# Performance work log

Measured on AMD Instinct MI355X. Metric: run time of the kernel, lower is better.

The kernel has to match this reference:

```python
import jax, jax.numpy as jnp
import numpy as np
import math

L, B, T, C, H, DH, V, MEM = 6, 2, 1024, 1024, 16, 64, 32000, 128

def _ln(x, g, b):
    m = jnp.mean(x, -1, keepdims=True)
    v = jnp.mean((x - m) ** 2, -1, keepdims=True)
    return (x - m) * jax.lax.rsqrt(v + 1e-5) * g + b

def _rel_shift(x):
    # x: [B,H,Q,K]; TransformerXL shift trick: pad zero col, reshape, drop first row
    b, h, q, k = x.shape
    xp = jnp.pad(x, ((0, 0), (0, 0), (0, 0), (1, 0)))
    xp = xp.reshape(b, h, k + 1, q)
    return xp[:, :, 1:, :].reshape(b, h, q, k)

def setup_inputs():
    key = jax.random.key(0)
    ks = jax.random.split(key, 12)
    d = {}
    d['idx'] = jax.random.randint(ks[0], (B, T), 0, V)
    d['mems'] = jax.random.normal(ks[1], (L, B, MEM, C), dtype=jnp.float32) * 0.02
    d['wte'] = jax.random.normal(ks[2], (V, C), dtype=jnp.float32) * 0.02
    d['ln1_g'] = jnp.ones((L, C), jnp.float32); d['ln1_b'] = jnp.zeros((L, C), jnp.float32)
    d['attn_w'] = jax.random.normal(ks[3], (L, C, 3 * C), dtype=jnp.float32) * 0.02
    d['attn_b'] = jnp.zeros((L, 3 * C), jnp.float32)
    d['proj_w'] = jax.random.normal(ks[4], (L, C, C), dtype=jnp.float32) * 0.02
    d['proj_b'] = jnp.zeros((L, C), jnp.float32)
    d['r_emb'] = jax.random.normal(ks[5], (L, H, DH), dtype=jnp.float32) * 0.02
    d['r_bias'] = jax.random.normal(ks[6], (L, H, DH), dtype=jnp.float32) * 0.02
    d['ln2_g'] = jnp.ones((L, C), jnp.float32); d['ln2_b'] = jnp.zeros((L, C), jnp.float32)
    d['fc_w'] = jax.random.normal(ks[7], (L, C, 4 * C), dtype=jnp.float32) * 0.02
    d['fc_b'] = jnp.zeros((L, 4 * C), jnp.float32)
    d['fc2_w'] = jax.random.normal(ks[8], (L, 4 * C, C), dtype=jnp.float32) * 0.02
    d['fc2_b'] = jnp.zeros((L, C), jnp.float32)
    d['lnf_g'] = jnp.ones((C,), jnp.float32); d['lnf_b'] = jnp.zeros((C,), jnp.float32)
    d['lm_w'] = jax.random.normal(ks[9], (C, V), dtype=jnp.float32) * 0.02
    return d

def _attn(x, mem, w, b, pw, pb, remb, rbias):
    Bx, Tx, Cx = x.shape
    cat = jnp.concatenate([mem, x], axis=1)          # [B,K,C], K = mem_len + Tx
    K = cat.shape[1]
    qkv = cat @ w + b
    q, k, v = jnp.split(qkv, 3, axis=-1)
    q = q.reshape(Bx, K, H, DH).transpose(0, 2, 1, 3)
    k = k.reshape(Bx, K, H, DH).transpose(0, 2, 1, 3)
    v = v.reshape(Bx, K, H, DH).transpose(0, 2, 1, 3)
    q = q + rbias[None, :, None, :]
    AC = jnp.einsum('bhid,bhjd->bhij', q, k)
    # BD: r is r_emb broadcast over positions, so q@r^T is constant over j
    s = jnp.einsum('bhid,hd->bhi', q, remb)
    BD = _rel_shift(jnp.broadcast_to(s[..., None], (Bx, H, K, K)))
    p = jax.nn.softmax((AC + BD) / math.sqrt(DH), axis=-1)
    y = jnp.einsum('bhij,bhjd->bhid', p, v).transpose(0, 2, 1, 3).reshape(Bx, K, Cx)
    y = y @ pw + pb
    new_mem = cat[:, -MEM:]
    return y, new_mem

def reference(idx, mems, wte, ln1_g, ln1_b, attn_w, attn_b, proj_w, proj_b, r_emb, r_bias, ln2_g, ln2_b, fc_w, fc_b, fc2_w, fc2_b, lnf_g, lnf_b, lm_w):
    x = wte[idx]                                      # [B,T,C]
    new_mems = []
    for l in range(L):
        h = _ln(x, ln1_g[l], ln1_b[l])
        y, nm = _attn(h, mems[l], attn_w[l], attn_b[l], proj_w[l], proj_b[l], r_emb[l], r_bias[l])
        h2 = _ln(y, ln2_g[l], ln2_b[l])
        m = jax.nn.gelu(h2 @ fc_w[l] + fc_b[l], approximate=False) @ fc2_w[l] + fc2_b[l]
        x = y + m                                     # note: residual onto attn output (length grows by MEM per layer)
        new_mems.append(nm)
    x = _ln(x, lnf_g, lnf_b)
    logits = x @ lm_w                                 # [B, L*MEM+T, V]
    return logits, jnp.stack(new_mems)
```

## Files before the change

### kernel.cpp

```cpp
#include <hip/hip_runtime.h>
#include <hip/hip_bf16.h>
#include <hip/hip_fp16.h>

#define LNUM 6
#define BB 2
#define TT 1024
#define CC 1024
#define HH 16
#define DHH 64
#define VV 32000
#define MM 128

typedef _Float16 f16;
typedef _Float16 f16x8 __attribute__((ext_vector_type(8)));
typedef float f32x4 __attribute__((ext_vector_type(4)));

__device__ __forceinline__ void g2lds16(const void* g, void* l) {
    __builtin_amdgcn_global_load_lds((const __attribute__((address_space(1))) void*)g,
                                     (__attribute__((address_space(3))) void*)l,
                                     16, 0, 0);
}

__device__ __forceinline__ float wred(float v) {
#pragma unroll
    for (int o = 32; o > 0; o >>= 1) v += __shfl_xor(v, o);
    return v;
}

__global__ __launch_bounds__(256)
void transpose_k(const float* __restrict__ W, f16* __restrict__ WT, int R, int Cc)
{
    __shared__ float tile[64][65];
    const size_t base = (size_t)blockIdx.z * R * Cc;
    const int c0 = blockIdx.x * 64, r0 = blockIdx.y * 64;
    const int tx = threadIdx.x & 15, ty = threadIdx.x >> 4;
#pragma unroll
    for (int i = 0; i < 4; ++i) {
        const int row = ty + i * 16;
        float4 v = *(const float4*)&W[base + (size_t)(r0 + row) * Cc + c0 + tx * 4];
        tile[row][tx * 4 + 0] = v.x;
        tile[row][tx * 4 + 1] = v.y;
        tile[row][tx * 4 + 2] = v.z;
        tile[row][tx * 4 + 3] = v.w;
    }
    __syncthreads();
#pragma unroll
    for (int i = 0; i < 4; ++i) {
        const int c = ty + i * 16;
        union { f16 h4[4]; uint2 u; } pk;
        pk.h4[0] = (f16)tile[tx * 4 + 0][c];
        pk.h4[1] = (f16)tile[tx * 4 + 1][c];
        pk.h4[2] = (f16)tile[tx * 4 + 2][c];
        pk.h4[3] = (f16)tile[tx * 4 + 3][c];
        *(uint2*)&WT[base + (size_t)(c0 + c) * R + r0 + tx * 4] = pk.u;
    }
}

__global__ __launch_bounds__(256)
void embed_k(const int* __restrict__ idx, const float* __restrict__ wte, float* __restrict__ X)
{
    const int row = blockIdx.x;
    const int id = idx[row];
    const float4* src = (const float4*)(wte + (size_t)id * CC);
    float4* dst = (float4*)(X + (size_t)row * CC);
    dst[threadIdx.x] = src[threadIdx.x];
}

__global__ __launch_bounds__(256)
void ln_k(const float* __restrict__ X, const float* __restrict__ g,
          const float* __restrict__ bta, f16* __restrict__ outH)
{
    const int row = blockIdx.x * 4 + (threadIdx.x >> 6);
    const int lane = threadIdx.x & 63;
    const float4* xr = (const float4*)(X + (size_t)row * CC);
    float4 v[4];
    float s = 0.f;
#pragma unroll
    for (int i = 0; i < 4; ++i) { v[i] = xr[i * 64 + lane]; s += v[i].x + v[i].y + v[i].z + v[i].w; }
    s = wred(s);
    const float mean = s * (1.f / CC);
    float q = 0.f;
#pragma unroll
    for (int i = 0; i < 4; ++i) {
        float a = v[i].x - mean, b = v[i].y - mean, c = v[i].z - mean, d = v[i].w - mean;
        q += a * a + b * b + c * c + d * d;
    }
    q = wred(q);
    const float rs = rsqrtf(q * (1.f / CC) + 1e-5f);
    const float4* g4 = (const float4*)g;
    const float4* b4 = (const float4*)bta;
    uint2* orow = (uint2*)(outH + (size_t)row * CC);
#pragma unroll
    for (int i = 0; i < 4; ++i) {
        float4 gg = g4[i * 64 + lane], bb = b4[i * 64 + lane];
        union { f16 h4[4]; uint2 u; } pk;
        pk.h4[0] = (f16)((v[i].x - mean) * rs * gg.x + bb.x);
        pk.h4[1] = (f16)((v[i].y - mean) * rs * gg.y + bb.y);
        pk.h4[2] = (f16)((v[i].z - mean) * rs * gg.z + bb.z);
        pk.h4[3] = (f16)((v[i].w - mean) * rs * gg.w + bb.w);
        orow[i * 64 + lane] = pk.u;
    }
}

__global__ __launch_bounds__(256)
void ln1cat_k(const float* __restrict__ X, const float* __restrict__ memsL,
              const float* __restrict__ g, const float* __restrict__ bta,
              f16* __restrict__ catH, float* __restrict__ nmOut,
              int K, int Kin)
{
    const int row = blockIdx.x * 4 + (threadIdx.x >> 6);
    const int lane = threadIdx.x & 63;
    const int b = row / K, rr = row % K;
    uint2* crow = (uint2*)(catH + (size_t)row * CC);
    if (rr < MM) {
        const float4* src = (const float4*)(memsL + ((size_t)b * MM + rr) * CC);
#pragma unroll
        for (int i = 0; i < 4; ++i) {
            float4 vv = src[i * 64 + lane];
            union { f16 h4[4]; uint2 u; } pk;
            pk.h4[0] = (f16)vv.x; pk.h4[1] = (f16)vv.y; pk.h4[2] = (f16)vv.z; pk.h4[3] = (f16)vv.w;
            crow[i * 64 + lane] = pk.u;
        }
        return;
    }
    const float4* xr = (const float4*)(X + ((size_t)b * Kin + (rr - MM)) * CC);
    float4 v[4];
    float s = 0.f;
#pragma unroll
    for (int i = 0; i < 4; ++i) { v[i] = xr[i * 64 + lane]; s += v[i].x + v[i].y + v[i].z + v[i].w; }
    s = wred(s);
    const float mean = s * (1.f / CC);
    float q = 0.f;
#pragma unroll
    for (int i = 0; i < 4; ++i) {
        float a = v[i].x - mean, b2 = v[i].y - mean, c = v[i].z - mean, d = v[i].w - mean;
        q += a * a + b2 * b2 + c * c + d * d;
    }
    q = wred(q);
    const float rs = rsqrtf(q * (1.f / CC) + 1e-5f);
    const float4* g4 = (const float4*)g;
    const float4* b4 = (const float4*)bta;
    float4* nm = nullptr;
    if (rr >= K - MM) nm = (float4*)(nmOut + ((size_t)b * MM + (rr - (K - MM))) * CC);
#pragma unroll
    for (int i = 0; i < 4; ++i) {
        float4 gg = g4[i * 64 + lane], bb = b4[i * 64 + lane];
        float4 o;
        o.x = (v[i].x - mean) * rs * gg.x + bb.x;
        o.y = (v[i].y - mean) * rs * gg.y + bb.y;
        o.z = (v[i].z - mean) * rs * gg.z + bb.z;
        o.w = (v[i].w - mean) * rs * gg.w + bb.w;
        union { f16 h4[4]; uint2 u; } pk;
        pk.h4[0] = (f16)o.x; pk.h4[1] = (f16)o.y; pk.h4[2] = (f16)o.z; pk.h4[3] = (f16)o.w;
        crow[i * 64 + lane] = pk.u;
        if (nm) nm[i * 64 + lane] = o;
    }
}

template <int EPI>
__global__ __launch_bounds__(256, 2)
void gemm_k(const f16* __restrict__ A, const f16* __restrict__ BT,
            const float* __restrict__ bias, const float* __restrict__ res,
            float* __restrict__ outF, f16* __restrict__ outH,
            int M, int N, int Kc)
{
    __shared__ f16 sA[2][128 * 32];
    __shared__ f16 sB[2][128 * 32];

    const int nbn = N >> 7;
    const int nwg = gridDim.x;
    const int id = blockIdx.x;
    const int qq = nwg >> 3, r8 = nwg & 7;
    const int xcd = id & 7, pos = id >> 3;
    const int wgid = (xcd < r8 ? xcd * (qq + 1) : r8 * (qq + 1) + (xcd - r8) * qq) + pos;
    const int bm = wgid / nbn, bn = wgid % nbn;

    const int tid = threadIdx.x;
    const int w = tid >> 6, l = tid & 63;
    const int wr = w >> 1, wc = w & 1;
    const int lr = l & 15, lk = (l >> 4) * 8;

    f32x4 acc[4][4] = {};

    const int ar = w * 32 + (l >> 2);
    const int ak = (l & 3) * 8;
    const f16* gA = A + (size_t)(bm * 128 + ar) * Kc + ak;
    const f16* gB = BT + (size_t)(bn * 128 + ar) * Kc + ak;

    auto stage = [&](int slot, int kt) {
        g2lds16(gA + kt, &sA[slot][w * 1024]);
        g2lds16(gA + kt + (size_t)16 * Kc, &sA[slot][w * 1024 + 512]);
        g2lds16(gB + kt, &sB[slot][w * 1024]);
        g2lds16(gB + kt + (size_t)16 * Kc, &sB[slot][w * 1024 + 512]);
    };

    stage(0, 0);
    asm volatile("s_waitcnt vmcnt(0)" ::: "memory");
    __builtin_amdgcn_s_barrier();

    int cur = 0;
    for (int kt = 0; kt < Kc; kt += 32) {
        if (kt + 32 < Kc) stage(cur ^ 1, kt + 32);
        f16x8 af[4], bf[4];
#pragma unroll
        for (int mi = 0; mi < 4; ++mi) af[mi] = *(const f16x8*)&sA[cur][(wr * 64 + mi * 16 + lr) * 32 + lk];
#pragma unroll
        for (int ni = 0; ni < 4; ++ni) bf[ni] = *(const f16x8*)&sB[cur][(wc * 64 + ni * 16 + lr) * 32 + lk];
        asm volatile("s_waitcnt lgkmcnt(0)" ::: "memory");
        __builtin_amdgcn_sched_barrier(0);
#pragma unroll
        for (int mi = 0; mi < 4; ++mi)
#pragma unroll
            for (int ni = 0; ni < 4; ++ni)
                acc[mi][ni] = __builtin_amdgcn_mfma_f32_16x16x32_f16(af[mi], bf[ni], acc[mi][ni], 0, 0, 0);
        asm volatile("s_waitcnt vmcnt(0)" ::: "memory");
        __builtin_amdgcn_s_barrier();
        cur ^= 1;
    }

    const int orow0 = bm * 128 + wr * 64 + (l >> 4) * 4;
    const int ocol0 = bn * 128 + wc * 64 + lr;
#pragma unroll
    for (int mi = 0; mi < 4; ++mi)
#pragma unroll
        for (int ni = 0; ni < 4; ++ni) {
            const int col = ocol0 + ni * 16;
            const float bv = (EPI >= 1) ? bias[col] : 0.f;
#pragma unroll
            for (int r = 0; r < 4; ++r) {
                const int row = orow0 + mi * 16 + r;
                float v = acc[mi][ni][r] + bv;
                if (EPI == 2) {
                    const float u = 1.5957691216057308f * (v + 0.044715f * v * v * v);
                    const float e = __expf(u);
                    v = v * e / (e + 1.f);
                    outH[(size_t)row * N + col] = (f16)v;
                } else if (EPI == 4) {
                    outH[(size_t)row * N + col] = (f16)v;
                } else if (EPI == 3) {
                    v += res[(size_t)row * N + col];
                    outF[(size_t)row * N + col] = v;
                } else {
                    outF[(size_t)row * N + col] = v;
                }
            }
        }
}

template <int EPI>
__global__ __launch_bounds__(512, 2)
void gemm256_k(const f16* __restrict__ A, const f16* __restrict__ BT,
               const float* __restrict__ bias,
               float* __restrict__ outF, f16* __restrict__ outH,
               int M, int N, int Kc)
{
    __shared__ char ldsbuf[131072];
    char* ldsA = ldsbuf;
    char* ldsB = ldsbuf + 65536;

    const int nbm = M >> 8;
    const int nwg = gridDim.x;
    int id = blockIdx.x;
    const int qq = nwg >> 3, rr8 = nwg & 7;
    const int xcd = id & 7, pos = id >> 3;
    const int wgid = (xcd < rr8 ? xcd * (qq + 1) : rr8 * (qq + 1) + (xcd - rr8) * qq) + pos;
    const int bm = wgid % nbm, bn = wgid / nbm;

    const int t_ = threadIdx.x;
    const int w = t_ >> 6, l = t_ & 63;
    const int wm = w >> 2, wn = w & 3;
    const int lr = l & 15, lhi = l >> 4;

    const f16* gA = A + (size_t)bm * 256 * Kc;
    const f16* gB = BT + (size_t)bn * 256 * Kc;

    auto stage = [&](const f16* Gbase, char* ldsHalf, int kt) {
#pragma unroll
        for (int ii = 0; ii < 2; ++ii) {
            const int gb = (w << 1) + ii;
            const int s = (gb << 6) + l;
            const int row = s >> 3, grp = s & 7;
            g2lds16(Gbase + (size_t)row * Kc + kt + ((grp ^ (row & 7)) << 3),
                    ldsHalf + gb * 1024);
        }
    };
    auto rdfrag = [&](const char* halfBase, int rowInHalf, int ks) -> f16x8 {
        return *(const f16x8*)(halfBase + rowInHalf * 128 +
                               ((((ks << 2) + lhi) ^ (rowInHalf & 7)) << 4));
    };

    f32x4 acc[8][4] = {};
    f16x8 aA[4][2], blo[2][2], bhi[2][2];

    const int NT = Kc >> 6;
    const char* aHalf0 = ldsA + wm * 16384;
    const char* aHalf1 = ldsA + 32768 + wm * 16384;
    const char* bHalf0 = ldsB + (wn >> 1) * 16384;
    const char* bHalf1 = ldsB + 32768 + (wn >> 1) * 16384;
    const int brow = (wn & 1) * 64;

    stage(gA, ldsA + 0, 0);
    stage(gA + (size_t)128 * Kc, ldsA + 16384, 0);
    stage(gB, ldsB + 0, 0);
    stage(gB + (size_t)128 * Kc, ldsB + 16384, 0);
    stage(gB, ldsB + 32768, 64);
    stage(gB + (size_t)128 * Kc, ldsB + 49152, 64);
    asm volatile("s_waitcnt vmcnt(0)" ::: "memory");
    __builtin_amdgcn_s_barrier();

#define MFMA_QUAD(MQ, NQ, BR)                                                            \
    __builtin_amdgcn_s_setprio(1);                                                       \
    _Pragma("unroll") for (int mf = 0; mf < 4; ++mf)                                     \
    _Pragma("unroll") for (int nf = 0; nf < 2; ++nf)                                     \
    _Pragma("unroll") for (int ks = 0; ks < 2; ++ks)                                     \
        acc[(MQ)*4 + mf][(NQ)*2 + nf] =                                                  \
            __builtin_amdgcn_mfma_f32_16x16x32_f16(aA[mf][ks], BR[nf][ks],               \
                                                   acc[(MQ)*4 + mf][(NQ)*2 + nf], 0, 0, 0); \
    __builtin_amdgcn_s_setprio(0);

#define PHASE_SYNC()                                          \
    __builtin_amdgcn_s_barrier();                             \
    asm volatile("s_waitcnt lgkmcnt(0)" ::: "memory");        \
    __builtin_amdgcn_sched_barrier(0);

    for (int t = 0; t < NT; t += 2) {
        const bool pf0 = (t + 2) < NT;
        const int kb = (t + 1) << 6, kc2 = (t + 2) << 6, kd = (t + 3) << 6;

#pragma unroll
        for (int mf = 0; mf < 4; ++mf)
#pragma unroll
            for (int ks = 0; ks < 2; ++ks) aA[mf][ks] = rdfrag(aHalf0, mf * 16 + lr, ks);
#pragma unroll
        for (int nf = 0; nf < 2; ++nf)
#pragma unroll
            for (int ks = 0; ks < 2; ++ks) blo[nf][ks] = rdfrag(bHalf0, brow + nf * 16 + lr, ks);
        stage(gA, ldsA + 32768, kb);
        PHASE_SYNC();
        MFMA_QUAD(0, 0, blo);
        __builtin_amdgcn_s_barrier();

#pragma unroll
        for (int nf = 0; nf < 2; ++nf)
#pragma unroll
            for (int ks = 0; ks < 2; ++ks) bhi[nf][ks] = rdfrag(bHalf0, brow + 32 + nf * 16 + lr, ks);
        stage(gA + (size_t)128 * Kc, ldsA + 49152, kb);
        PHASE_SYNC();
        MFMA_QUAD(0, 1, bhi);
        __builtin_amdgcn_s_barrier();

#pragma unroll
        for (int mf = 0; mf < 4; ++mf)
#pragma unroll
            for (int ks = 0; ks < 2; ++ks) aA[mf][ks] = rdfrag(aHalf0, 64 + mf * 16 + lr, ks);
        if (pf0) stage(gB, ldsB + 0, kc2);
        PHASE_SYNC();
        MFMA_QUAD(1, 0, blo);
        __builtin_amdgcn_s_barrier();

        if (pf0) {
            stage(gB + (size_t)128 * Kc, ldsB + 16384, kc2);
            asm volatile("s_waitcnt vmcnt(4)" ::: "memory");
        } else {
            asm volatile("s_waitcnt vmcnt(0)" ::: "memory");
        }
        PHASE_SYNC();
        MFMA_QUAD(1, 1, bhi);
        __builtin_amdgcn_s_barrier();

#pragma unroll
        for (int mf = 0; mf < 4; ++mf)
#pragma unroll
            for (int ks = 0; ks < 2; ++ks) aA[mf][ks] = rdfrag(aHalf1, mf * 16 + lr, ks);
#pragma unroll
        for (int nf = 0; nf < 2; ++nf)
#pragma unroll
            for (int ks = 0; ks < 2; ++ks) blo[nf][ks] = rdfrag(bHalf1, brow + nf * 16 + lr, ks);
        if (pf0) stage(gA, ldsA + 0, kc2);
        PHASE_SYNC();
        MFMA_QUAD(0, 0, blo);
        __builtin_amdgcn_s_barrier();

#pragma unroll
        for (int nf = 0; nf < 2; ++nf)
#pragma unroll
            for (int ks = 0; ks < 2; ++ks) bhi[nf][ks] = rdfrag(bHalf1, brow + 32 + nf * 16 + lr, ks);
        if (pf0) stage(gA + (size_t)128 * Kc, ldsA + 16384, kc2);
        PHASE_SYNC();
        MFMA_QUAD(0, 1, bhi);
        __builtin_amdgcn_s_barrier();

#pragma unroll
        for (int mf = 0; mf < 4; ++mf)
#pragma unroll
            for (int ks = 0; ks < 2; ++ks) aA[mf][ks] = rdfrag(aHalf1, 64 + mf * 16 + lr, ks);
        if (pf0) stage(gB, ldsB + 32768, kd);
        PHASE_SYNC();
        MFMA_QUAD(1, 0, blo);
        __builtin_amdgcn_s_barrier();

        if (pf0) {
            stage(gB + (size_t)128 * Kc, ldsB + 49152, kd);
            asm volatile("s_waitcnt vmcnt(4)" ::: "memory");
        } else {
            asm volatile("s_waitcnt vmcnt(0)" ::: "memory");
        }
        PHASE_SYNC();
        MFMA_QUAD(1, 1, bhi);
        __builtin_amdgcn_s_barrier();
    }
#undef MFMA_QUAD
#undef PHASE_SYNC

    const int rb0 = bm * 256 + wm * 128 + lhi * 4;
    const int cb0 = bn * 256 + wn * 64 + lr;
#pragma unroll
    for (int mf = 0; mf < 8; ++mf)
#pragma unroll
        for (int nf = 0; nf < 4; ++nf) {
            const int col = cb0 + nf * 16;
            const float bv = (EPI >= 1) ? bias[col] : 0.f;
#pragma unroll
            for (int r = 0; r < 4; ++r) {
                const int row = rb0 + mf * 16 + r;
                float v = acc[mf][nf][r] + bv;
                if (EPI == 2) {
                    const float u = 1.5957691216057308f * (v + 0.044715f * v * v * v);
                    const float e = __expf(u);
                    v = v * e / (e + 1.f);
                    outH[(size_t)row * N + col] = (f16)v;
                } else if (EPI == 4) {
                    outH[(size_t)row * N + col] = (f16)v;
                } else {
                    __builtin_nontemporal_store(v, &outF[(size_t)row * N + col]);
                }
            }
        }
}

__global__ __launch_bounds__(256)
void attn_k(const f16* __restrict__ qkv, const float* __restrict__ remb,
            const float* __restrict__ rbias, f16* __restrict__ yH, int K)
{
    __shared__ f16 K_lds[2][64 * 64];
    __shared__ f16 Vt_lds[2][64 * 64];
    __shared__ f16 P_lds[64 * 64];
    __shared__ float s_s[66];

    const int b = blockIdx.x >> 4, h = blockIdx.x & 15;
    const int i0 = blockIdx.y * 64;
    const int t = threadIdx.x;
    const int w = t >> 6, l = t & 63;
    const int c = l & 15, g = l >> 4;

    const f16* qg = qkv + (size_t)b * K * 3072 + h * 64;
    const f16* kg = qg + 1024;
    const f16* vg = qg + 2048;
    const float* rb = rbias + h * 64;
    const float* re = remb + h * 64;

    const int kb = t >> 4, db = t & 15;

    auto stageK = [&](int j0, int slot) {
#pragma unroll
        for (int i = 0; i < 2; ++i) {
            const int s = w * 128 + i * 64 + l;
            const int row = s >> 3, grp = s & 7;
            g2lds16(kg + (size_t)(j0 + row) * 3072 + ((grp ^ (row & 7)) * 8),
                    (char*)K_lds[slot] + (size_t)(w * 128 + i * 64) * 16);
        }
    };
    auto loadV = [&](int j0, uint2* rowv) {
#pragma unroll
        for (int i = 0; i < 4; ++i)
            rowv[i] = *(const uint2*)(vg + (size_t)(j0 + kb * 4 + i) * 3072 + db * 4);
    };
    auto writeVt = [&](const uint2* rowvu, int slot) {
#pragma unroll
        for (int j = 0; j < 4; ++j) {
            union { uint2 u; f16 hh[4]; } colv;
#pragma unroll
            for (int i = 0; i < 4; ++i) {
                union { uint2 u; f16 hh[4]; } rv; rv.u = rowvu[i];
                colv.hh[i] = rv.hh[j];
            }
            const int d = db * 4 + j;
            *(uint2*)((char*)Vt_lds[slot] + d * 128 + ((kb * 8) ^ ((d & 7) << 4))) = colv.u;
        }
    };

    f16x8 qf[2];
    {
        const int qrow = i0 + w * 16 + c;
#pragma unroll
        for (int ks = 0; ks < 2; ++ks) {
            f16x8 raw = *(const f16x8*)(qg + (size_t)qrow * 3072 + ks * 32 + g * 8);
            f16x8 o;
#pragma unroll
            for (int j = 0; j < 8; ++j) o[j] = (f16)((float)raw[j] + rb[ks * 32 + g * 8 + j]);
            qf[ks] = o;
        }
    }
    if (t < 65) {
        float sv = 0.f;
        const int i = i0 + t;
        if (i < K) {
            const f16* qr = qg + (size_t)i * 3072;
#pragma unroll
            for (int d8 = 0; d8 < 8; ++d8) {
                f16x8 v8 = *(const f16x8*)(qr + d8 * 8);
#pragma unroll
                for (int j = 0; j < 8; ++j) sv += ((float)v8[j] + rb[d8 * 8 + j]) * re[d8 * 8 + j];
            }
        }
        s_s[t] = sv;
    }

    {
        uint2 rowv[4];
        stageK(0, 0);
        loadV(0, rowv);
        writeVt(rowv, 0);
    }
    __syncthreads();

    float sA[4], sB[4];
#pragma unroll
    for (int r = 0; r < 4; ++r) {
        sA[r] = s_s[w * 16 + g * 4 + r];
        sB[r] = s_s[w * 16 + g * 4 + r + 1];
    }

    float m_run[4] = {0.f, 0.f, 0.f, 0.f};
    float psum[4] = {0.f, 0.f, 0.f, 0.f};
    f32x4 yacc[4] = {};

    int cur = 0;
    for (int j0 = 0; j0 < K; j0 += 64, cur ^= 1) {
        const bool more = (j0 + 64) < K;
        uint2 rowv[4];
        if (more) { stageK(j0 + 64, cur ^ 1); loadV(j0 + 64, rowv); }

        f32x4 sc[4] = {};
#pragma unroll
        for (int tt = 0; tt < 4; ++tt) {
            const int row = tt * 16 + c;
#pragma unroll
            for (int ks = 0; ks < 2; ++ks) {
                f16x8 kf = *(const f16x8*)((char*)K_lds[cur] + row * 128 + ((ks * 64 + g * 16) ^ ((row & 7) << 4)));
                sc[tt] = __builtin_amdgcn_mfma_f32_16x16x32_f16(qf[ks], kf, sc[tt], 0, 0, 0);
            }
        }

        float p[4][4];
#pragma unroll
        for (int tt = 0; tt < 4; ++tt)
#pragma unroll
            for (int r = 0; r < 4; ++r) {
                const int gi = i0 + w * 16 + g * 4 + r;
                const int gj = j0 + tt * 16 + c;
                const float bd = (gj <= gi) ? sA[r] : ((gj == gi + 1) ? 0.f : sB[r]);
                p[tt][r] = (sc[tt][r] + bd) * 0.125f;
            }

        float lmax[4];
        bool need = false;
#pragma unroll
        for (int r = 0; r < 4; ++r) {
            lmax[r] = fmaxf(fmaxf(p[0][r], p[1][r]), fmaxf(p[2][r], p[3][r]));
            need |= (lmax[r] > m_run[r] + 8.f);
        }
        if (__any(need)) {
#pragma unroll
            for (int r = 0; r < 4; ++r) {
                float mx = lmax[r];
                mx = fmaxf(mx, __shfl_xor(mx, 1));
                mx = fmaxf(mx, __shfl_xor(mx, 2));
                mx = fmaxf(mx, __shfl_xor(mx, 4));
                mx = fmaxf(mx, __shfl_xor(mx, 8));
                if (mx > m_run[r]) {
                    const float f = __expf(m_run[r] - mx);
                    m_run[r] = mx;
                    psum[r] *= f;
#pragma unroll
                    for (int tt = 0; tt < 4; ++tt) yacc[tt][r] *= f;
                }
            }
        }
#pragma unroll
        for (int r = 0; r < 4; ++r) {
            float ss = 0.f;
#pragma unroll
            for (int tt = 0; tt < 4; ++tt) {
                const float e = __expf(p[tt][r] - m_run[r]);
                p[tt][r] = e;
                ss += e;
            }
            psum[r] += ss;
        }

        if (more) writeVt(rowv, cur ^ 1);
#pragma unroll
        for (int tt = 0; tt < 4; ++tt)
#pragma unroll
            for (int r = 0; r < 4; ++r) {
                const int q = w * 16 + g * 4 + r;
                *(f16*)((char*)P_lds + q * 128 + (((tt * 16 + c) * 2) ^ ((q & 7) << 4))) = (f16)p[tt][r];
            }
        asm volatile("s_waitcnt lgkmcnt(0)" ::: "memory");
        __builtin_amdgcn_sched_barrier(0);

        {
            const int qrow = w * 16 + c;
            f16x8 pa[2];
#pragma unroll
            for (int ks = 0; ks < 2; ++ks)
                pa[ks] = *(const f16x8*)((char*)P_lds + qrow * 128 + ((ks * 64 + g * 16) ^ ((qrow & 7) << 4)));
#pragma unroll
            for (int tt = 0; tt < 4; ++tt) {
                const int drow = tt * 16 + c;
#pragma unroll
                for (int ks = 0; ks < 2; ++ks) {
                    f16x8 vb = *(const f16x8*)((char*)Vt_lds[cur] + drow * 128 + ((ks * 64 + g * 16) ^ ((drow & 7) << 4)));
                    yacc[tt] = __builtin_amdgcn_mfma_f32_16x16x32_f16(pa[ks], vb, yacc[tt], 0, 0, 0);
                }
            }
        }
        __syncthreads();
    }

#pragma unroll
    for (int r = 0; r < 4; ++r) {
        float ps = psum[r];
        ps += __shfl_xor(ps, 1);
        ps += __shfl_xor(ps, 2);
        ps += __shfl_xor(ps, 4);
        ps += __shfl_xor(ps, 8);
        const float inv = 1.f / ps;
        const int row = i0 + w * 16 + g * 4 + r;
        f16* dst = yH + (size_t)(b * K + row) * CC + h * 64;
#pragma unroll
        for (int tt = 0; tt < 4; ++tt)
            dst[tt * 16 + c] = (f16)(yacc[tt][r] * inv);
    }
}

extern "C" void kernel_launch(void* const* d_in, const int* in_sizes, int n_in,
                              void* d_out, int out_size, void* d_ws, size_t ws_size,
                              hipStream_t stream)
{
    (void)in_sizes; (void)n_in; (void)out_size; (void)ws_size;
    const int*   idx    = (const int*)  d_in[0];
    const float* mems   = (const float*)d_in[1];
    const float* wte    = (const float*)d_in[2];
    const float* ln1_g  = (const float*)d_in[3];
    const float* ln1_b  = (const float*)d_in[4];
    const float* attn_w = (const float*)d_in[5];
    const float* attn_b = (const float*)d_in[6];
    const float* proj_w = (const float*)d_in[7];
    const float* proj_b = (const float*)d_in[8];
    const float* r_emb  = (const float*)d_in[9];
    const float* r_bias = (const float*)d_in[10];
    const float* ln2_g  = (const float*)d_in[11];
    const float* ln2_b  = (const float*)d_in[12];
    const float* fc_w   = (const float*)d_in[13];
    const float* fc_b   = (const float*)d_in[14];
    const float* fc2_w  = (const float*)d_in[15];
    const float* fc2_b  = (const float*)d_in[16];
    const float* lnf_g  = (const float*)d_in[17];
    const float* lnf_b  = (const float*)d_in[18];
    const float* lm_w   = (const float*)d_in[19];
    float* out = (float*)d_out;

    char* wp = (char*)d_ws; size_t off = 0;
    auto carve = [&](size_t bytes) -> void* {
        void* p = wp + off; off += (bytes + 255) & ~(size_t)255; return p;
    };
    const int KMAX = TT + LNUM * MM;
    f16*  attn_wT = (f16*) carve((size_t)LNUM * 3 * CC * CC * 2);
    f16*  proj_wT = (f16*) carve((size_t)LNUM * CC * CC * 2);
    f16*  fc_wT   = (f16*) carve((size_t)LNUM * 4 * CC * CC * 2);
    f16*  fc2_wT  = (f16*) carve((size_t)LNUM * 4 * CC * CC * 2);
    f16*  lm_wT   = (f16*) carve((size_t)VV * CC * 2);
    float* x0     = (float*)carve((size_t)BB * KMAX * CC * 4);
    float* x1     = (float*)carve((size_t)BB * KMAX * CC * 4);
    f16*  catH    = (f16*) carve((size_t)BB * KMAX * CC * 2);
    f16*  qkv16   = (f16*) carve((size_t)BB * KMAX * 3 * CC * 2);
    f16*  yH      = (f16*) carve((size_t)BB * KMAX * CC * 2);
    float* yp     = (float*)carve((size_t)BB * KMAX * CC * 4);
    f16*  h2H     = (f16*) carve((size_t)BB * KMAX * CC * 2);
    f16*  a1H     = (f16*) carve((size_t)BB * KMAX * 4 * CC * 2);
    f16*  xfH     = (f16*) carve((size_t)BB * KMAX * CC * 2);

    transpose_k<<<dim3(3 * CC / 64, CC / 64, LNUM), 256, 0, stream>>>(attn_w, attn_wT, CC, 3 * CC);
    transpose_k<<<dim3(CC / 64, CC / 64, LNUM),     256, 0, stream>>>(proj_w, proj_wT, CC, CC);
    transpose_k<<<dim3(4 * CC / 64, CC / 64, LNUM), 256, 0, stream>>>(fc_w, fc_wT, CC, 4 * CC);
    transpose_k<<<dim3(CC / 64, 4 * CC / 64, LNUM), 256, 0, stream>>>(fc2_w, fc2_wT, 4 * CC, CC);
    transpose_k<<<dim3(VV / 64, CC / 64, 1),        256, 0, stream>>>(lm_w, lm_wT, CC, VV);

    embed_k<<<BB * TT, 256, 0, stream>>>(idx, wte, x0);

    const size_t LOGITS = (size_t)BB * KMAX * VV;
    float* xcur = x0; float* xnxt = x1;
    for (int l = 0; l < LNUM; ++l) {
        const int Kin = TT + MM * l;
        const int K = Kin + MM;
        const int Mrows = BB * K;
        const int nbm128 = Mrows / 128;
        ln1cat_k<<<Mrows / 4, 256, 0, stream>>>(xcur, mems + (size_t)l * BB * MM * CC,
                                                ln1_g + l * CC, ln1_b + l * CC,
                                                catH, out + LOGITS + (size_t)l * BB * MM * CC, K, Kin);
        gemm_k<4><<<(3 * CC / 128) * nbm128, 256, 0, stream>>>(
            catH, attn_wT + (size_t)l * 3 * CC * CC, attn_b + (size_t)l * 3 * CC, nullptr,
            nullptr, qkv16, Mrows, 3 * CC, CC);
        attn_k<<<dim3(BB * HH, K / 64), 256, 0, stream>>>(
            qkv16, r_emb + (size_t)l * HH * DHH, r_bias + (size_t)l * HH * DHH, yH, K);
        gemm_k<1><<<(CC / 128) * nbm128, 256, 0, stream>>>(
            yH, proj_wT + (size_t)l * CC * CC, proj_b + (size_t)l * CC, nullptr,
            yp, nullptr, Mrows, CC, CC);
        ln_k<<<Mrows / 4, 256, 0, stream>>>(yp, ln2_g + l * CC, ln2_b + l * CC, h2H);
        gemm_k<2><<<(4 * CC / 128) * nbm128, 256, 0, stream>>>(
            h2H, fc_wT + (size_t)l * 4 * CC * CC, fc_b + (size_t)l * 4 * CC, nullptr,
            nullptr, a1H, Mrows, 4 * CC, CC);
        gemm_k<3><<<(CC / 128) * nbm128, 256, 0, stream>>>(
            a1H, fc2_wT + (size_t)l * 4 * CC * CC, fc2_b + (size_t)l * CC, yp,
            xnxt, nullptr, Mrows, CC, 4 * CC);
        float* tmp = xcur; xcur = xnxt; xnxt = tmp;
    }
    ln_k<<<(BB * KMAX) / 4, 256, 0, stream>>>(xcur, lnf_g, lnf_b, xfH);
    gemm256_k<0><<<(BB * KMAX / 256) * (VV / 256), 512, 0, stream>>>(
        xfH, lm_wT, nullptr, out, nullptr, BB * KMAX, VV, CC);
}
```

Before: 2.029 ms.

## Deepen gemm K-tile to 64 with XOR-swizzled LDS layout

The 128x128 gemm kernel now stages 64-wide K slices instead of 32. This halves the number of barrier and wait iterations and doubles the MFMA work issued per sync. LDS rows are XOR-swizzled by row to avoid bank conflicts on the wider rows. LDS use doubles to 64KB per block, which may limit the two-blocks-per-CU occupancy target. The large-tile kernel's fp32 output also switches from nontemporal to normal stores.

```diff
diff --git a/kernel.cpp b/kernel.cpp
--- a/kernel.cpp
+++ b/kernel.cpp
@@ -164,8 +164,8 @@
             float* __restrict__ outF, f16* __restrict__ outH,
             int M, int N, int Kc)
 {
-    __shared__ f16 sA[2][128 * 32];
-    __shared__ f16 sB[2][128 * 32];
+    __shared__ f16 sA[2][128 * 64];
+    __shared__ f16 sB[2][128 * 64];
 
     const int nbn = N >> 7;
     const int nwg = gridDim.x;
@@ -178,20 +178,22 @@
     const int tid = threadIdx.x;
     const int w = tid >> 6, l = tid & 63;
     const int wr = w >> 1, wc = w & 1;
-    const int lr = l & 15, lk = (l >> 4) * 8;
+    const int lr = l & 15, lhi = l >> 4;
 
     f32x4 acc[4][4] = {};
 
-    const int ar = w * 32 + (l >> 2);
-    const int ak = (l & 3) * 8;
-    const f16* gA = A + (size_t)(bm * 128 + ar) * Kc + ak;
-    const f16* gB = BT + (size_t)(bn * 128 + ar) * Kc + ak;
+    const f16* gA = A + (size_t)(bm * 128) * Kc;
+    const f16* gB = BT + (size_t)(bn * 128) * Kc;
 
     auto stage = [&](int slot, int kt) {
-        g2lds16(gA + kt, &sA[slot][w * 1024]);
-        g2lds16(gA + kt + (size_t)16 * Kc, &sA[slot][w * 1024 + 512]);
-        g2lds16(gB + kt, &sB[slot][w * 1024]);
-        g2lds16(gB + kt + (size_t)16 * Kc, &sB[slot][w * 1024 + 512]);
+#pragma unroll
+        for (int p = 0; p < 4; ++p) {
+            const int s = p * 256 + tid;
+            const int row = s >> 3, gr = s & 7;
+            const int srcoff = (gr ^ (row & 7)) << 3;
+            g2lds16(gA + (size_t)row * Kc + kt + srcoff, &sA[slot][s * 8]);
+            g2lds16(gB + (size_t)row * Kc + kt + srcoff, &sB[slot][s * 8]);
+        }
     };
 
     stage(0, 0);
@@ -199,20 +201,32 @@
     __builtin_amdgcn_s_barrier();
 
     int cur = 0;
-    for (int kt = 0; kt < Kc; kt += 32) {
-        if (kt + 32 < Kc) stage(cur ^ 1, kt + 32);
-        f16x8 af[4], bf[4];
-#pragma unroll
-        for (int mi = 0; mi < 4; ++mi) af[mi] = *(const f16x8*)&sA[cur][(wr * 64 + mi * 16 + lr) * 32 + lk];
-#pragma unroll
-        for (int ni = 0; ni < 4; ++ni) bf[ni] = *(const f16x8*)&sB[cur][(wc * 64 + ni * 16 + lr) * 32 + lk];
+    for (int kt = 0; kt < Kc; kt += 64) {
+        if (kt + 64 < Kc) stage(cur ^ 1, kt + 64);
+        f16x8 af[4][2], bf[4][2];
+#pragma unroll
+        for (int mi = 0; mi < 4; ++mi)
+#pragma unroll
+            for (int ks = 0; ks < 2; ++ks) {
+                const int r = wr * 64 + mi * 16 + lr;
+                af[mi][ks] = *(const f16x8*)&sA[cur][r * 64 + ((((ks << 2) + lhi) ^ (r & 7)) << 3)];
+            }
+#pragma unroll
+        for (int ni = 0; ni < 4; ++ni)
+#pragma unroll
+            for (int ks = 0; ks < 2; ++ks) {
+                const int r = wc * 64 + ni * 16 + lr;
+                bf[ni][ks] = *(const f16x8*)&sB[cur][r * 64 + ((((ks << 2) + lhi) ^ (r & 7)) << 3)];
+            }
         asm volatile("s_waitcnt lgkmcnt(0)" ::: "memory");
         __builtin_amdgcn_sched_barrier(0);
 #pragma unroll
         for (int mi = 0; mi < 4; ++mi)
 #pragma unroll
             for (int ni = 0; ni < 4; ++ni)
-                acc[mi][ni] = __builtin_amdgcn_mfma_f32_16x16x32_f16(af[mi], bf[ni], acc[mi][ni], 0, 0, 0);
+#pragma unroll
+                for (int ks = 0; ks < 2; ++ks)
+                    acc[mi][ni] = __builtin_amdgcn_mfma_f32_16x16x32_f16(af[mi][ks], bf[ni][ks], acc[mi][ni], 0, 0, 0);
         asm volatile("s_waitcnt vmcnt(0)" ::: "memory");
         __builtin_amdgcn_s_barrier();
         cur ^= 1;
@@ -432,7 +446,7 @@
                 } else if (EPI == 4) {
                     outH[(size_t)row * N + col] = (f16)v;
                 } else {
-                    __builtin_nontemporal_store(v, &outF[(size_t)row * N + col]);
+                    outF[(size_t)row * N + col] = v;
                 }
             }
         }
```

Result: no change. 2.025 ms (-0.2%).
